# Performance work log

Hardware: AMD Instinct MI355X
Metric: run time of the kernel (lower is better)

The kernel has to match this reference:

```python
import jax, jax.numpy as jnp
import numpy as np

TOP_K = 8
N_EXPERTS = 64
HIDDEN = 4096


def setup_inputs() -> dict:
    key = jax.random.key(0)
    k1, k2 = jax.random.split(key)
    hidden_states = jax.random.normal(k1, (4, 4096, HIDDEN), dtype=jnp.float32)
    # kaiming_uniform_(a=sqrt(5)) on a (64, 4096) weight -> U(-b, b), b = sqrt(6/((1+5)*4096)) = 1/sqrt(4096)
    bound = 1.0 / np.sqrt(HIDDEN)
    weight = jax.random.uniform(k2, (N_EXPERTS, HIDDEN), dtype=jnp.float32,
                                minval=-bound, maxval=bound)
    return {"hidden_states": hidden_states, "weight": weight}


def reference(hidden_states, weight):
    bsz, seq_len, h = hidden_states.shape
    x = hidden_states.reshape(-1, h)                       # [T, H]
    logits = jnp.einsum('th,eh->te', x, weight)            # [T, E]
    scores = jax.nn.softmax(logits, axis=-1)
    topk_weight, topk_idx = jax.lax.top_k(scores, TOP_K)   # [T, K]
    denom = jnp.sum(topk_weight, axis=-1, keepdims=True) + 1e-20
    topk_weight = topk_weight / denom
    topk_weight = topk_weight.reshape(bsz, seq_len, TOP_K)
    topk_idx = topk_idx.reshape(bsz, seq_len, TOP_K)
    # training-time aux loss (seq_aux path): histogram of argmax expert * mean prob
    probs = scores                                         # softmax(logits)
    top1 = jnp.argmax(probs, axis=-1)                      # [T]
    counts = jnp.zeros((N_EXPERTS,), dtype=jnp.float32).at[top1].add(1.0)
    route_prob = jnp.mean(probs, axis=0)                   # [E]
    route_frac = counts / jnp.sum(counts)
    aux_loss = jnp.sum(route_prob * route_frac) * N_EXPERTS
    return topk_idx, topk_weight, aux_loss
```

## Files before the change

### kernel.cpp

```cpp
#include <hip/hip_runtime.h>
#include <hip/hip_bf16.h>

#define TOKS 16384
#define HID  4096
#define NEXP 64
#define EPS  1e-4f

#define WS_FLAGCNT  128
#define WS_FLAGLIST 192
#define WS_BPACK    16576

typedef __attribute__((ext_vector_type(8))) short short8_t;
typedef __attribute__((ext_vector_type(4))) float f32x4;

static __device__ __forceinline__ unsigned short f2bf_rn(float x) {
    unsigned u = __builtin_bit_cast(unsigned, x);
    u = (u + 0x7fffu + ((u >> 16) & 1u)) >> 16;
    return (unsigned short)u;
}
static __device__ __forceinline__ float bf2f(unsigned short h) {
    return __builtin_bit_cast(float, (unsigned)h << 16);
}
static __device__ __forceinline__ void gl2lds16(const void* g, void* l) {
    __builtin_amdgcn_global_load_lds(
        (const __attribute__((address_space(1))) unsigned int*)g,
        (__attribute__((address_space(3))) unsigned int*)l, 16, 0, 0);
}

__global__ void moe_prep(const float* __restrict__ W, unsigned short* __restrict__ Bpk,
                         float* __restrict__ wsf) {
    const int idx = blockIdx.x * blockDim.x + threadIdx.x;
    if (idx < 192) wsf[idx] = 0.0f;
    if (idx >= NEXP * HID) return;
    const int n = idx >> 12;
    const int k = idx & 4095;
    const float w = W[idx];
    const unsigned short hi = f2bf_rn(w);
    const unsigned short lo = f2bf_rn(w - bf2f(hi));
    const int kt   = k >> 5;
    const int nt   = n >> 4;
    const int lane = (n & 15) | (((k >> 3) & 3) << 4);
    const int j    = k & 7;
    const int dst  = (((kt << 2) + nt) << 10) + (lane << 3) + j;
    Bpk[dst]       = hi;
    Bpk[dst + 512] = lo;
}

__global__ __launch_bounds__(256, 2)
void moe_fused(const float* __restrict__ X, const unsigned short* __restrict__ Bpk,
               float* __restrict__ out, float* __restrict__ wsf) {
    __shared__ __align__(16) char xraw[2][9216];
    __shared__ __align__(16) unsigned short bs[2][8192];
    float (*L)[68] = (float (*)[68])&xraw[0][0];

    const int tid  = threadIdx.x;
    const int lane = tid & 63;
    const int w    = tid >> 6;
    const int mt   = w & 1;
    const int nh   = w >> 1;
    const int g    = lane >> 4;
    const int tok0 = blockIdx.x * 32;

    f32x4 acc[2];
    acc[0] = (f32x4){0.f, 0.f, 0.f, 0.f};
    acc[1] = (f32x4){0.f, 0.f, 0.f, 0.f};

    int xlds[3]; size_t xsrc[3];
    #pragma unroll
    for (int i = 0; i < 3; ++i) {
        int t = w + 4 * i; if (t > 8) t = w;
        const int byte  = t * 1024 + (lane << 4);
        int row = byte / 272;
        const int inrow = byte - row * 272;
        int col = (inrow < 256) ? (inrow >> 2) : 0;
        if (row > 31) { row = 31; col = 0; }
        xlds[i] = t * 1024;
        xsrc[i] = (size_t)(tok0 + row) * HID + col;
    }

    #define STAGE(bf, ss)                                                              \
    {                                                                                  \
        const int k0_ = (ss) << 6;                                                     \
        _Pragma("unroll")                                                              \
        for (int i = 0; i < 3; ++i)                                                    \
            gl2lds16(X + xsrc[i] + k0_, (void*)(&xraw[bf][0] + xlds[i]));              \
        _Pragma("unroll")                                                              \
        for (int j = 0; j < 4; ++j) {                                                  \
            const int t = (w << 2) + j;                                                \
            gl2lds16((const char*)Bpk + ((size_t)(ss) << 14) + (t << 10) + (lane << 4), \
                     (void*)((char*)&bs[bf][0] + (t << 10)));                          \
        }                                                                              \
    }

    STAGE(0, 0);
    asm volatile("s_waitcnt vmcnt(0)" ::: "memory");
    __syncthreads();

    const int tr = (mt << 4) + (lane & 15);
    int cur = 0;

    for (int s = 0; s < 64; ++s) {
        if (s < 63) STAGE(cur ^ 1, s + 1);

        const char* ab = &xraw[cur][0] + tr * 272;
        const char* bb = (const char*)&bs[cur][0];
        #pragma unroll
        for (int ktl = 0; ktl < 2; ++ktl) {
            const float4 a0 = *(const float4*)(ab + ktl * 128 + g * 32);
            const float4 a1 = *(const float4*)(ab + ktl * 128 + g * 32 + 16);
            const float xv[8] = {a0.x, a0.y, a0.z, a0.w, a1.x, a1.y, a1.z, a1.w};
            short8_t ah, al;
            #pragma unroll
            for (int j = 0; j < 8; ++j) {
                const unsigned u = __builtin_bit_cast(unsigned, xv[j]);
                ah[j] = (short)(u >> 16);
                const float hif = __builtin_bit_cast(float, u & 0xFFFF0000u);
                al[j] = (short)(__builtin_bit_cast(unsigned, xv[j] - hif) >> 16);
            }
            #pragma unroll
            for (int ntl = 0; ntl < 2; ++ntl) {
                const char* bp = bb + (((ktl << 2) + (nh << 1) + ntl) << 11) + (lane << 4);
                const short8_t bh = *(const short8_t*)bp;
                const short8_t bl = *(const short8_t*)(bp + 1024);
                acc[ntl] = __builtin_amdgcn_mfma_f32_16x16x32_bf16(ah, bh, acc[ntl], 0, 0, 0);
                acc[ntl] = __builtin_amdgcn_mfma_f32_16x16x32_bf16(al, bh, acc[ntl], 0, 0, 0);
                acc[ntl] = __builtin_amdgcn_mfma_f32_16x16x32_bf16(ah, bl, acc[ntl], 0, 0, 0);
            }
        }
        __syncthreads();
        cur ^= 1;
    }

    #pragma unroll
    for (int ntl = 0; ntl < 2; ++ntl)
        #pragma unroll
        for (int r = 0; r < 4; ++r)
            L[(mt << 4) + (g << 2) + r][(nh << 5) + (ntl << 4) + (lane & 15)] = acc[ntl][r];
    __syncthreads();

    float* outIdx = out;
    float* outW   = out + TOKS * 8;
    int* flagcnt  = (int*)wsf + WS_FLAGCNT;
    int* flaglist = (int*)wsf + WS_FLAGLIST;

    float rp = 0.f;
    #pragma unroll
    for (int tt = 0; tt < 8; ++tt) {
        const int tl = (w << 3) + tt;
        const float lg = L[tl][lane];

        float v = lg; int idx = lane;
        #pragma unroll
        for (int size = 2; size <= 64; size <<= 1) {
            #pragma unroll
            for (int str = size >> 1; str > 0; str >>= 1) {
                const float ov = __shfl_xor(v, str, 64);
                const int   oi = __shfl_xor(idx, str, 64);
                const bool pb = (ov > v) || (ov == v && oi < idx);
                const bool keepFirst = ((lane & str) == 0) == ((lane & size) == 0);
                if (pb == keepFirst) { v = ov; idx = oi; }
            }
        }

        const float m = __shfl(v, 0, 64);
        const float p = __expf(lg - m);
        float sdenom = p;
        #pragma unroll
        for (int o = 32; o; o >>= 1) sdenom += __shfl_xor(sdenom, o, 64);
        const float inv_s = 1.0f / sdenom;
        rp += p * inv_s;

        const float wkv = __expf(v - m) * inv_s;
        float d8 = (lane < 8) ? wkv : 0.f;
        #pragma unroll
        for (int o = 1; o < 8; o <<= 1) d8 += __shfl_xor(d8, o, 64);
        const float invd = 1.0f / (d8 + 1e-20f);
        const float nv = __shfl_down(v, 1, 64);
        const bool flg = __any(lane < 8 && (v - nv) < EPS);

        const int gtok = tok0 + tl;
        if (lane < 8) {
            outIdx[(size_t)gtok * 8 + lane] = (float)idx;
            outW[(size_t)gtok * 8 + lane]   = wkv * invd;
        }
        if (lane == 0) {
            atomicAdd(&wsf[NEXP + idx], 1.0f);
            if (flg) {
                const int pos = atomicAdd(flagcnt, 1);
                if (pos < TOKS) flaglist[pos] = gtok;
            }
        }
    }
    atomicAdd(&wsf[lane], rp);
    #undef STAGE
}

__global__ __launch_bounds__(256, 2)
void moe_fix(const float* __restrict__ X, const float* __restrict__ W,
             float* __restrict__ out, float* __restrict__ wsf) {
    __shared__ double red[256];
    const int tid = threadIdx.x;
    const int e   = tid & 63;
    const int kc  = tid >> 6;
    const int nf  = min(*((int*)wsf + WS_FLAGCNT), TOKS);
    const int* flaglist = (const int*)wsf + WS_FLAGLIST;
    float* outIdx = out;
    float* outW   = out + TOKS * 8;

    for (int fi = blockIdx.x; fi < nf; fi += gridDim.x) {
        const int tok = flaglist[fi];
        const float* xrow = X + (size_t)tok * HID + kc * 1024;
        const float* wrow = W + (size_t)e  * HID + kc * 1024;
        double part = 0.0;
        for (int j = 0; j < 1024; j += 4) {
            const float4 xv = *(const float4*)(xrow + j);
            const float4 wv = *(const float4*)(wrow + j);
            part = fma((double)xv.x, (double)wv.x, part);
            part = fma((double)xv.y, (double)wv.y, part);
            part = fma((double)xv.z, (double)wv.z, part);
            part = fma((double)xv.w, (double)wv.w, part);
        }
        red[tid] = part;
        __syncthreads();
        if (tid < 64) {
            const double lg = ((red[tid] + red[64 + tid]) + red[128 + tid]) + red[192 + tid];
            const float lgf = (float)lg;
            float m = lgf;
            #pragma unroll
            for (int o = 32; o; o >>= 1) m = fmaxf(m, __shfl_xor(m, o, 64));
            const float p = __expf(lgf - m);
            float s = p;
            #pragma unroll
            for (int o = 32; o; o >>= 1) s += __shfl_xor(s, o, 64);
            const float inv_s = 1.0f / s;

            double v = lg;
            double bw[8]; int ik[8];
            #pragma unroll
            for (int k = 0; k < 8; ++k) {
                double bv = v; int bi = tid;
                #pragma unroll
                for (int o = 32; o; o >>= 1) {
                    const double ov = __shfl_xor(bv, o, 64);
                    const int    oi = __shfl_xor(bi, o, 64);
                    if (ov > bv || (ov == bv && oi < bi)) { bv = ov; bi = oi; }
                }
                bw[k] = bv; ik[k] = bi;
                if (tid == bi) v = -1.0e300;
            }
            float wk[8]; float denom = 1e-20f;
            #pragma unroll
            for (int k = 0; k < 8; ++k) {
                wk[k] = __expf((float)bw[k] - m) * inv_s; denom += wk[k];
            }
            const float invd = 1.0f / denom;
            const size_t base = (size_t)tok * 8;
            const int oldtop = (int)outIdx[base];
            if (tid < 8) {
                outIdx[base + tid] = (float)ik[tid];
                outW[base + tid]   = wk[tid] * invd;
            }
            if (tid == 0 && ik[0] != oldtop) {
                atomicAdd(&wsf[NEXP + oldtop], -1.0f);
                atomicAdd(&wsf[NEXP + ik[0]],  1.0f);
            }
        }
        __syncthreads();
    }
}

__global__ void moe_final(const float* __restrict__ wsf, float* __restrict__ out) {
    const int e = threadIdx.x;
    float v = wsf[e] * wsf[NEXP + e];
    #pragma unroll
    for (int o = 32; o; o >>= 1) v += __shfl_xor(v, o, 64);
    if (e == 0)
        out[2 * TOKS * 8] = v * (64.0f / ((float)TOKS * (float)TOKS));
}

__global__ void moe_init(float* __restrict__ wsf, int n) {
    const int i = blockIdx.x * blockDim.x + threadIdx.x;
    if (i < n) wsf[i] = 0.0f;
}

__global__ void moe_w_cvt(const float* __restrict__ W, double* __restrict__ Wd) {
    const int i = blockIdx.x * blockDim.x + threadIdx.x;
    if (i < NEXP * HID) Wd[i] = (double)W[i];
}

__global__ __launch_bounds__(512, 2)
void moe_mono(const float* __restrict__ X, const double* __restrict__ Wd,
              float* __restrict__ out, float* __restrict__ wsf) {
    __shared__ double xs[64][66];
    __shared__ double L2[64][65];
    const int tid  = threadIdx.x;
    const int lane = tid & 63;
    const int wid  = __builtin_amdgcn_readfirstlane(tid >> 6);
    const int tok0 = blockIdx.x * 64;
    double acc[8] = {0., 0., 0., 0., 0., 0., 0., 0.};
    for (int h0 = 0; h0 < HID; h0 += 64) {
        #pragma unroll
        for (int i = 0; i < 8; ++i) {
            const int li = tid + i * 512;
            xs[li >> 6][li & 63] = (double)X[((size_t)(tok0 + (li >> 6)) << 12) + (h0 + (li & 63))];
        }
        __syncthreads();
        const double* wchunk = Wd + (((size_t)(wid << 3)) << 12) + h0;
        #pragma unroll 2
        for (int hh = 0; hh < 64; hh += 2) {
            const double2 xv = *(const double2*)&xs[lane][hh];
            #pragma unroll
            for (int e = 0; e < 8; ++e) {
                const double* wr = wchunk + (((size_t)e) << 12) + hh;
                acc[e] = fma(xv.x, wr[0], acc[e]);
                acc[e] = fma(xv.y, wr[1], acc[e]);
            }
        }
        __syncthreads();
    }
    #pragma unroll
    for (int e = 0; e < 8; ++e) L2[lane][(wid << 3) + e] = acc[e];
    __syncthreads();
    float* outIdx = out;
    float* outW   = out + (TOKS * 8);
    float rp = 0.0f;
    for (int tt = 0; tt < 8; ++tt) {
        const int t = (wid << 3) + tt;
        const double lg = L2[t][lane];
        const float lgf = (float)lg;
        float m = lgf;
        #pragma unroll
        for (int o = 32; o; o >>= 1) m = fmaxf(m, __shfl_xor(m, o, 64));
        const float p = __expf(lgf - m);
        float s = p;
        #pragma unroll
        for (int o = 32; o; o >>= 1) s += __shfl_xor(s, o, 64);
        const float inv_s = 1.0f / s;
        rp += p * inv_s;
        double v = lg;
        float wk[8]; int ik[8];
        #pragma unroll
        for (int k = 0; k < 8; ++k) {
            double bv = v; int bi = lane;
            #pragma unroll
            for (int o = 32; o; o >>= 1) {
                const double ov = __shfl_xor(bv, o, 64);
                const int    oi = __shfl_xor(bi, o, 64);
                if (ov > bv || (ov == bv && oi < bi)) { bv = ov; bi = oi; }
            }
            wk[k] = __expf((float)bv - m) * inv_s; ik[k] = bi;
            if (lane == bi) v = -1.0e300;
        }
        if (lane == 0) {
            const float denom = (((wk[0]+wk[1])+(wk[2]+wk[3])) +
                                 ((wk[4]+wk[5])+(wk[6]+wk[7]))) + 1e-20f;
            const float invd = 1.0f / denom;
            const size_t base = ((size_t)(tok0 + t)) << 3;
            #pragma unroll
            for (int k = 0; k < 8; ++k) {
                outIdx[base + k] = (float)ik[k];
                outW[base + k]   = wk[k] * invd;
            }
            atomicAdd(&wsf[NEXP + ik[0]], 1.0f);
        }
    }
    atomicAdd(&wsf[lane], rp);
}

extern "C" void kernel_launch(void* const* d_in, const int* in_sizes, int n_in,
                              void* d_out, int out_size, void* d_ws, size_t ws_size,
                              hipStream_t stream) {
    const float* X = (const float*)d_in[0];
    const float* W = (const float*)d_in[1];
    float* out = (float*)d_out;
    float* wsf = (float*)d_ws;

    const size_t need = 4ull * WS_BPACK + 2ull * 524288;

    if (ws_size >= need) {
        unsigned short* Bpk = (unsigned short*)(wsf + WS_BPACK);
        moe_prep<<<(NEXP * HID + 255) / 256, 256, 0, stream>>>(W, Bpk, wsf);
        moe_fused<<<TOKS / 32, 256, 0, stream>>>(X, Bpk, out, wsf);
        moe_fix<<<256, 256, 0, stream>>>(X, W, out, wsf);
        moe_final<<<1, 64, 0, stream>>>(wsf, out);
    } else {
        double* Wd = (double*)d_ws;
        float* wsf2 = (float*)(Wd + NEXP * HID);
        moe_w_cvt<<<(NEXP * HID + 255) / 256, 256, 0, stream>>>(W, Wd);
        moe_init<<<1, 256, 0, stream>>>(wsf2, 128);
        moe_mono<<<TOKS / 64, 512, 0, stream>>>(X, Wd, out, wsf2);
        moe_final<<<1, 64, 0, stream>>>(wsf2, out);
    }
}
```

Baseline: 239.9 us.

## Split K across two blocks and move top-k into a separate kernel

The fused GEMM+routing kernel is split into a GEMM kernel with 64-token tiles, 512 threads, and a K dimension split across two grid slices, each writing partial logits to workspace. A new topk kernel sums the two partials and performs the softmax, top-k and aux accumulation. The goal is more blocks and larger tiles to raise parallelism and bandwidth use during the X-streaming GEMM. The cost is an extra kernel launch plus a round trip of partial logits through global memory.

```diff
diff --git a/kernel.cpp b/kernel.cpp
--- a/kernel.cpp
+++ b/kernel.cpp
@@ -9,6 +9,7 @@
 #define WS_FLAGCNT  128
 #define WS_FLAGLIST 192
 #define WS_BPACK    16576
+#define WS_PBASE    278720
 
 typedef __attribute__((ext_vector_type(8))) short short8_t;
 typedef __attribute__((ext_vector_type(4))) float f32x4;
@@ -46,20 +47,22 @@
     Bpk[dst + 512] = lo;
 }
 
-__global__ __launch_bounds__(256, 2)
-void moe_fused(const float* __restrict__ X, const unsigned short* __restrict__ Bpk,
-               float* __restrict__ out, float* __restrict__ wsf) {
-    __shared__ __align__(16) char xraw[2][9216];
+__global__ __launch_bounds__(512, 2)
+void moe_gemm(const float* __restrict__ X, const unsigned short* __restrict__ Bpk,
+              float* __restrict__ P) {
+    __shared__ __align__(16) char xraw[2][17408];
     __shared__ __align__(16) unsigned short bs[2][8192];
     float (*L)[68] = (float (*)[68])&xraw[0][0];
 
     const int tid  = threadIdx.x;
     const int lane = tid & 63;
     const int w    = tid >> 6;
-    const int mt   = w & 1;
-    const int nh   = w >> 1;
+    const int mt   = w & 3;
+    const int nh   = w >> 2;
     const int g    = lane >> 4;
-    const int tok0 = blockIdx.x * 32;
+    const int tok0 = blockIdx.x * 64;
+    const int kc   = blockIdx.y;
+    const int gs0  = kc << 5;
 
     f32x4 acc[2];
     acc[0] = (f32x4){0.f, 0.f, 0.f, 0.f};
@@ -68,39 +71,38 @@
     int xlds[3]; size_t xsrc[3];
     #pragma unroll
     for (int i = 0; i < 3; ++i) {
-        int t = w + 4 * i; if (t > 8) t = w;
-        const int byte  = t * 1024 + (lane << 4);
-        int row = byte / 272;
-        const int inrow = byte - row * 272;
-        int col = (inrow < 256) ? (inrow >> 2) : 0;
-        if (row > 31) { row = 31; col = 0; }
+        int t = w * 3 + i; if (t >= 17) t -= 17;
+        const int off = t * 1024 + (lane << 4);
+        const int row = off / 272;
+        const int rb  = off - row * 272;
+        const int col = (rb < 256) ? (rb >> 2) : 0;
         xlds[i] = t * 1024;
         xsrc[i] = (size_t)(tok0 + row) * HID + col;
     }
 
-    #define STAGE(bf, ss)                                                              \
+    #define STAGE(bf, gss)                                                             \
     {                                                                                  \
-        const int k0_ = (ss) << 6;                                                     \
+        const int k0_ = (gss) << 6;                                                    \
         _Pragma("unroll")                                                              \
         for (int i = 0; i < 3; ++i)                                                    \
             gl2lds16(X + xsrc[i] + k0_, (void*)(&xraw[bf][0] + xlds[i]));              \
         _Pragma("unroll")                                                              \
-        for (int j = 0; j < 4; ++j) {                                                  \
-            const int t = (w << 2) + j;                                                \
-            gl2lds16((const char*)Bpk + ((size_t)(ss) << 14) + (t << 10) + (lane << 4), \
-                     (void*)((char*)&bs[bf][0] + (t << 10)));                          \
+        for (int j = 0; j < 2; ++j) {                                                  \
+            const int c1k = (w << 1) + j;                                              \
+            gl2lds16((const char*)Bpk + ((size_t)(gss) << 14) + (c1k << 10) + (lane << 4), \
+                     (void*)((char*)&bs[bf][0] + (c1k << 10)));                        \
         }                                                                              \
     }
 
-    STAGE(0, 0);
+    STAGE(0, gs0);
     asm volatile("s_waitcnt vmcnt(0)" ::: "memory");
     __syncthreads();
 
     const int tr = (mt << 4) + (lane & 15);
     int cur = 0;
 
-    for (int s = 0; s < 64; ++s) {
-        if (s < 63) STAGE(cur ^ 1, s + 1);
+    for (int s = 0; s < 32; ++s) {
+        if (s < 31) STAGE(cur ^ 1, gs0 + s + 1);
 
         const char* ab = &xraw[cur][0] + tr * 272;
         const char* bb = (const char*)&bs[cur][0];
@@ -137,7 +139,24 @@
         for (int r = 0; r < 4; ++r)
             L[(mt << 4) + (g << 2) + r][(nh << 5) + (ntl << 4) + (lane & 15)] = acc[ntl][r];
     __syncthreads();
-
+    {
+        const int row = tid >> 3;
+        const int c0  = (tid & 7) << 3;
+        float* dst = P + ((size_t)kc * TOKS + tok0 + row) * NEXP + c0;
+        const float* src = &L[row][c0];
+        *(float4*)dst       = *(const float4*)src;
+        *(float4*)(dst + 4) = *(const float4*)(src + 4);
+    }
+    #undef STAGE
+}
+
+__global__ __launch_bounds__(256, 4)
+void moe_topk(const float* __restrict__ P, float* __restrict__ out,
+              float* __restrict__ wsf) {
+    const int tid  = threadIdx.x;
+    const int lane = tid & 63;
+    const int wid  = tid >> 6;
+    const int tok0 = blockIdx.x * 16;
     float* outIdx = out;
     float* outW   = out + TOKS * 8;
     int* flagcnt  = (int*)wsf + WS_FLAGCNT;
@@ -145,9 +164,10 @@
 
     float rp = 0.f;
     #pragma unroll
-    for (int tt = 0; tt < 8; ++tt) {
-        const int tl = (w << 3) + tt;
-        const float lg = L[tl][lane];
+    for (int tt = 0; tt < 4; ++tt) {
+        const int tok = tok0 + wid * 4 + tt;
+        const float lg = P[(size_t)tok * NEXP + lane]
+                       + P[(size_t)(TOKS + tok) * NEXP + lane];
 
         float v = lg; int idx = lane;
         #pragma unroll
@@ -178,21 +198,19 @@
         const float nv = __shfl_down(v, 1, 64);
         const bool flg = __any(lane < 8 && (v - nv) < EPS);
 
-        const int gtok = tok0 + tl;
         if (lane < 8) {
-            outIdx[(size_t)gtok * 8 + lane] = (float)idx;
-            outW[(size_t)gtok * 8 + lane]   = wkv * invd;
+            outIdx[(size_t)tok * 8 + lane] = (float)idx;
+            outW[(size_t)tok * 8 + lane]   = wkv * invd;
         }
         if (lane == 0) {
             atomicAdd(&wsf[NEXP + idx], 1.0f);
             if (flg) {
                 const int pos = atomicAdd(flagcnt, 1);
-                if (pos < TOKS) flaglist[pos] = gtok;
+                if (pos < TOKS) flaglist[pos] = tok;
             }
         }
     }
     atomicAdd(&wsf[lane], rp);
-    #undef STAGE
 }
 
 __global__ __launch_bounds__(256, 2)
@@ -375,12 +393,15 @@
     float* out = (float*)d_out;
     float* wsf = (float*)d_ws;
 
-    const size_t need = 4ull * WS_BPACK + 2ull * 524288;
+    const size_t need = 4ull * (WS_PBASE + 2ull * TOKS * NEXP);
 
     if (ws_size >= need) {
         unsigned short* Bpk = (unsigned short*)(wsf + WS_BPACK);
+        float* P = wsf + WS_PBASE;
         moe_prep<<<(NEXP * HID + 255) / 256, 256, 0, stream>>>(W, Bpk, wsf);
-        moe_fused<<<TOKS / 32, 256, 0, stream>>>(X, Bpk, out, wsf);
+        dim3 g1(TOKS / 64, 2);
+        moe_gemm<<<g1, 512, 0, stream>>>(X, Bpk, P);
+        moe_topk<<<TOKS / 16, 256, 0, stream>>>(P, out, wsf);
         moe_fix<<<256, 256, 0, stream>>>(X, W, out, wsf);
         moe_final<<<1, 64, 0, stream>>>(wsf, out);
     } else {
```

Result: no change. 239.6 us (-0.2%).

## Split-K across warps with per-warp private LDS pipelines, no block barriers

Applied to the files above, without the earlier changes.

Each block now handles 16 tokens with 8 warps. The K dimension is split in two halves across warp pairs, and each warp owns a private LDS double buffer that it fills itself, waiting with vmcnt instead of __syncthreads in the main loop. Partial accumulators are reduced through LDS at the end. This removes per-step block-wide barriers and raises the number of blocks in flight. The cost is that each warp loads its own redundant copy of the X tile (four warps share the same tokens), and LDS use grows to 144KB per block, which limits occupancy to one block per CU.

```diff
diff --git a/kernel.cpp b/kernel.cpp
--- a/kernel.cpp
+++ b/kernel.cpp
@@ -46,96 +46,99 @@
     Bpk[dst + 512] = lo;
 }
 
-__global__ __launch_bounds__(256, 2)
+__global__ __launch_bounds__(512, 1)
 void moe_fused(const float* __restrict__ X, const unsigned short* __restrict__ Bpk,
                float* __restrict__ out, float* __restrict__ wsf) {
-    __shared__ __align__(16) char xraw[2][9216];
-    __shared__ __align__(16) unsigned short bs[2][8192];
-    float (*L)[68] = (float (*)[68])&xraw[0][0];
+    __shared__ __align__(16) char lds[8][18432];
+    float (*L)[68] = (float (*)[68])&lds[0][0];
 
     const int tid  = threadIdx.x;
     const int lane = tid & 63;
     const int w    = tid >> 6;
-    const int mt   = w & 1;
-    const int nh   = w >> 1;
+    const int kc   = w & 1;
+    const int nt   = w >> 1;
     const int g    = lane >> 4;
-    const int tok0 = blockIdx.x * 32;
-
-    f32x4 acc[2];
-    acc[0] = (f32x4){0.f, 0.f, 0.f, 0.f};
-    acc[1] = (f32x4){0.f, 0.f, 0.f, 0.f};
-
-    int xlds[3]; size_t xsrc[3];
+    const int tok0 = blockIdx.x * 16;
+    char* wb = &lds[w][0];
+
+    f32x4 acc = (f32x4){0.f, 0.f, 0.f, 0.f};
+
+    int xlds[5]; size_t xsrc[5];
     #pragma unroll
-    for (int i = 0; i < 3; ++i) {
-        int t = w + 4 * i; if (t > 8) t = w;
-        const int byte  = t * 1024 + (lane << 4);
+    for (int i = 0; i < 5; ++i) {
+        const int byte = i * 1024 + (lane << 4);
         int row = byte / 272;
         const int inrow = byte - row * 272;
         int col = (inrow < 256) ? (inrow >> 2) : 0;
-        if (row > 31) { row = 31; col = 0; }
-        xlds[i] = t * 1024;
+        if (row > 15) { row = 15; col = 0; }
+        xlds[i] = i * 1024;
         xsrc[i] = (size_t)(tok0 + row) * HID + col;
     }
 
-    #define STAGE(bf, ss)                                                              \
+    #define STAGE(bf, gs)                                                              \
     {                                                                                  \
-        const int k0_ = (ss) << 6;                                                     \
+        const int k0_ = (gs) << 6;                                                     \
         _Pragma("unroll")                                                              \
-        for (int i = 0; i < 3; ++i)                                                    \
-            gl2lds16(X + xsrc[i] + k0_, (void*)(&xraw[bf][0] + xlds[i]));              \
+        for (int i = 0; i < 5; ++i)                                                    \
+            gl2lds16(X + xsrc[i] + k0_, (void*)(wb + (bf) * 5120 + xlds[i]));          \
         _Pragma("unroll")                                                              \
         for (int j = 0; j < 4; ++j) {                                                  \
-            const int t = (w << 2) + j;                                                \
-            gl2lds16((const char*)Bpk + ((size_t)(ss) << 14) + (t << 10) + (lane << 4), \
-                     (void*)((char*)&bs[bf][0] + (t << 10)));                          \
+            const int kt_ = ((gs) << 1) + (j >> 1);                                    \
+            gl2lds16((const char*)Bpk + (((size_t)((kt_ << 2) + nt)) << 11)            \
+                         + ((j & 1) << 10) + (lane << 4),                              \
+                     (void*)(wb + 10240 + (bf) * 4096 + (j >> 1) * 2048 + ((j & 1) << 10))); \
         }                                                                              \
     }
 
-    STAGE(0, 0);
+    #define COMPUTE(bf)                                                                \
+    {                                                                                  \
+        const char* ab = wb + (bf) * 5120 + (lane & 15) * 272;                         \
+        const char* bb = wb + 10240 + (bf) * 4096;                                     \
+        _Pragma("unroll")                                                              \
+        for (int ktl = 0; ktl < 2; ++ktl) {                                            \
+            const float4 a0 = *(const float4*)(ab + ktl * 128 + g * 32);               \
+            const float4 a1 = *(const float4*)(ab + ktl * 128 + g * 32 + 16);          \
+            const float xv[8] = {a0.x, a0.y, a0.z, a0.w, a1.x, a1.y, a1.z, a1.w};      \
+            short8_t ah, al;                                                           \
+            _Pragma("unroll")                                                          \
+            for (int j = 0; j < 8; ++j) {                                              \
+                const unsigned u = __builtin_bit_cast(unsigned, xv[j]);                \
+                ah[j] = (short)(u >> 16);                                              \
+                const float hif = __builtin_bit_cast(float, u & 0xFFFF0000u);          \
+                al[j] = (short)(__builtin_bit_cast(unsigned, xv[j] - hif) >> 16);      \
+            }                                                                          \
+            const short8_t bh = *(const short8_t*)(bb + ktl * 2048 + (lane << 4));     \
+            const short8_t bl = *(const short8_t*)(bb + ktl * 2048 + 1024 + (lane << 4)); \
+            acc = __builtin_amdgcn_mfma_f32_16x16x32_bf16(ah, bh, acc, 0, 0, 0);       \
+            acc = __builtin_amdgcn_mfma_f32_16x16x32_bf16(al, bh, acc, 0, 0, 0);       \
+            acc = __builtin_amdgcn_mfma_f32_16x16x32_bf16(ah, bl, acc, 0, 0, 0);       \
+        }                                                                              \
+    }
+
+    const int gsbase = kc << 5;
+    STAGE(0, gsbase);
+    for (int s = 0; s < 31; ++s) {
+        STAGE((s + 1) & 1, gsbase + s + 1);
+        asm volatile("s_waitcnt vmcnt(9)" ::: "memory");
+        __builtin_amdgcn_sched_barrier(0);
+        COMPUTE(s & 1);
+    }
     asm volatile("s_waitcnt vmcnt(0)" ::: "memory");
+    __builtin_amdgcn_sched_barrier(0);
+    COMPUTE(1);
+
     __syncthreads();
-
-    const int tr = (mt << 4) + (lane & 15);
-    int cur = 0;
-
-    for (int s = 0; s < 64; ++s) {
-        if (s < 63) STAGE(cur ^ 1, s + 1);
-
-        const char* ab = &xraw[cur][0] + tr * 272;
-        const char* bb = (const char*)&bs[cur][0];
-        #pragma unroll
-        for (int ktl = 0; ktl < 2; ++ktl) {
-            const float4 a0 = *(const float4*)(ab + ktl * 128 + g * 32);
-            const float4 a1 = *(const float4*)(ab + ktl * 128 + g * 32 + 16);
-            const float xv[8] = {a0.x, a0.y, a0.z, a0.w, a1.x, a1.y, a1.z, a1.w};
-            short8_t ah, al;
-            #pragma unroll
-            for (int j = 0; j < 8; ++j) {
-                const unsigned u = __builtin_bit_cast(unsigned, xv[j]);
-                ah[j] = (short)(u >> 16);
-                const float hif = __builtin_bit_cast(float, u & 0xFFFF0000u);
-                al[j] = (short)(__builtin_bit_cast(unsigned, xv[j] - hif) >> 16);
-            }
-            #pragma unroll
-            for (int ntl = 0; ntl < 2; ++ntl) {
-                const char* bp = bb + (((ktl << 2) + (nh << 1) + ntl) << 11) + (lane << 4);
-                const short8_t bh = *(const short8_t*)bp;
-                const short8_t bl = *(const short8_t*)(bp + 1024);
-                acc[ntl] = __builtin_amdgcn_mfma_f32_16x16x32_bf16(ah, bh, acc[ntl], 0, 0, 0);
-                acc[ntl] = __builtin_amdgcn_mfma_f32_16x16x32_bf16(al, bh, acc[ntl], 0, 0, 0);
-                acc[ntl] = __builtin_amdgcn_mfma_f32_16x16x32_bf16(ah, bl, acc[ntl], 0, 0, 0);
-            }
-        }
-        __syncthreads();
-        cur ^= 1;
-    }
-
-    #pragma unroll
-    for (int ntl = 0; ntl < 2; ++ntl)
+    if (kc == 0) {
         #pragma unroll
         for (int r = 0; r < 4; ++r)
-            L[(mt << 4) + (g << 2) + r][(nh << 5) + (ntl << 4) + (lane & 15)] = acc[ntl][r];
+            L[(g << 2) + r][(nt << 4) + (lane & 15)] = acc[r];
+    }
+    __syncthreads();
+    if (kc == 1) {
+        #pragma unroll
+        for (int r = 0; r < 4; ++r)
+            L[(g << 2) + r][(nt << 4) + (lane & 15)] += acc[r];
+    }
     __syncthreads();
 
     float* outIdx = out;
@@ -145,8 +148,8 @@
 
     float rp = 0.f;
     #pragma unroll
-    for (int tt = 0; tt < 8; ++tt) {
-        const int tl = (w << 3) + tt;
+    for (int tt = 0; tt < 2; ++tt) {
+        const int tl = (w << 1) + tt;
         const float lg = L[tl][lane];
 
         float v = lg; int idx = lane;
@@ -193,6 +196,7 @@
     }
     atomicAdd(&wsf[lane], rp);
     #undef STAGE
+    #undef COMPUTE
 }
 
 __global__ __launch_bounds__(256, 2)
@@ -380,7 +384,7 @@
     if (ws_size >= need) {
         unsigned short* Bpk = (unsigned short*)(wsf + WS_BPACK);
         moe_prep<<<(NEXP * HID + 255) / 256, 256, 0, stream>>>(W, Bpk, wsf);
-        moe_fused<<<TOKS / 32, 256, 0, stream>>>(X, Bpk, out, wsf);
+        moe_fused<<<TOKS / 16, 512, 0, stream>>>(X, Bpk, out, wsf);
         moe_fix<<<256, 256, 0, stream>>>(X, W, out, wsf);
         moe_final<<<1, 64, 0, stream>>>(wsf, out);
     } else {
```

Result: slower. 294.0 us (+22.5%).
